# Kernel optimization log

Hardware: AMD Instinct MI355X
Metric: run time of the kernel (lower is better)

The kernel has to match this reference:

```python
import jax, jax.numpy as jnp
import numpy as np

C = 64          # in_channels (per-head channel dim)
HEADS = 8
GROUPS = 32
EPS = 1e-6
B, H, W = 8, 64, 64


def group_norm(x, gamma, beta):
    b, c, h, w = x.shape
    xg = x.reshape(b, GROUPS, c // GROUPS, h, w)
    mu = xg.mean(axis=(2, 3, 4), keepdims=True)
    var = xg.var(axis=(2, 3, 4), keepdims=True)
    xn = ((xg - mu) / jnp.sqrt(var + EPS)).reshape(b, c, h, w)
    return xn * gamma[None, :, None, None] + beta[None, :, None, None]


def conv1x1(x, wgt, bias):
    # wgt: [out_c, in_c], x: [b, in_c, h, w]
    return jnp.einsum('oc,bchw->bohw', wgt, x) + bias[None, :, None, None]


def setup_inputs() -> dict:
    key = jax.random.key(0)
    ks = jax.random.split(key, 10)
    sc_in = 1.0 / np.sqrt(C)
    sc_out = 1.0 / np.sqrt(C * HEADS)
    return {
        'x': jax.random.normal(ks[0], (B, C, H, W), dtype=jnp.float32),
        'gn_gamma': jnp.ones((C,), dtype=jnp.float32),
        'gn_beta': jnp.zeros((C,), dtype=jnp.float32),
        'Wq': jax.random.uniform(ks[1], (C * HEADS, C), jnp.float32, -sc_in, sc_in),
        'bq': jax.random.uniform(ks[2], (C * HEADS,), jnp.float32, -sc_in, sc_in),
        'Wk': jax.random.uniform(ks[3], (C * HEADS, C), jnp.float32, -sc_in, sc_in),
        'bk': jax.random.uniform(ks[4], (C * HEADS,), jnp.float32, -sc_in, sc_in),
        'Wv': jax.random.uniform(ks[5], (C * HEADS, C), jnp.float32, -sc_in, sc_in),
        'bv': jax.random.uniform(ks[6], (C * HEADS,), jnp.float32, -sc_in, sc_in),
        'Wo': jax.random.uniform(ks[7], (C, C * HEADS), jnp.float32, -sc_out, sc_out),
        'bo': jax.random.uniform(ks[8], (C,), jnp.float32, -sc_out, sc_out),
    }


def reference(x, gn_gamma, gn_beta, Wq, bq, Wk, bk, Wv, bv, Wo, bo):
    b, c, h, w = x.shape
    xn = group_norm(x, gn_gamma, gn_beta)
    # 1x1 conv projections -> [b, heads, c, h*w]
    q = conv1x1(xn, Wq, bq).reshape(b, HEADS, c, h * w)
    k = conv1x1(xn, Wk, bk).reshape(b, HEADS, c, h * w)
    v = conv1x1(xn, Wv, bv).reshape(b, HEADS, c, h * w)
    q = jax.nn.softmax(q, axis=-1)
    k = jax.nn.softmax(k, axis=-1)
    # out[b,h,c,q] = sum_k sum_p Q[b,h,p,q] K[b,h,p,k] V[b,h,c,k] / sqrt(c)
    # associativity: contract K with V first (O(hw*c^2) instead of O(hw^2*c))
    s = jnp.einsum('bhpk,bhck->bhpc', k, v)          # [b, heads, c, c]
    out = jnp.einsum('bhpq,bhpc->bhcq', q, s) / jnp.sqrt(jnp.float32(c))
    out = out.reshape(b, HEADS * c, h, w)
    return conv1x1(out, Wo, bo)
```

## Files before the change

kernel.cpp:

```cpp
#include <hip/hip_runtime.h>
#include <math.h>

#define BATCH 8
#define CH 64
#define NHEADS 8
#define NPIX 4096
#define QROWS 512

typedef __attribute__((ext_vector_type(8))) short short8v;
typedef __attribute__((ext_vector_type(16))) float f32x16;

__device__ inline float wave_sum(float v) {
#pragma unroll
    for (int off = 32; off; off >>= 1) v += __shfl_down(v, off, 64);
    return v;
}

__device__ inline void split_bf16(float f, short& h, short& l) {
    unsigned u = __float_as_uint(f);
    unsigned r = u + 0x7FFFu + ((u >> 16) & 1u);
    h = (short)(r >> 16);
    float hf = __uint_as_float(r & 0xFFFF0000u);
    float lf = f - hf;
    unsigned u2 = __float_as_uint(lf);
    unsigned r2 = u2 + 0x7FFFu + ((u2 >> 16) & 1u);
    l = (short)(r2 >> 16);
}

__device__ inline void split4(const float4 v, uint2& hi, uint2& lo) {
    short h0, h1, h2, h3, l0, l1, l2, l3;
    split_bf16(v.x, h0, l0); split_bf16(v.y, h1, l1);
    split_bf16(v.z, h2, l2); split_bf16(v.w, h3, l3);
    hi.x = (unsigned short)h0 | ((unsigned)(unsigned short)h1 << 16);
    hi.y = (unsigned short)h2 | ((unsigned)(unsigned short)h3 << 16);
    lo.x = (unsigned short)l0 | ((unsigned)(unsigned short)l1 << 16);
    lo.y = (unsigned short)l2 | ((unsigned)(unsigned short)l3 << 16);
}

__global__ __launch_bounds__(256) void gn_zero_kernel(
    const float* __restrict__ x, const float* __restrict__ gamma,
    const float* __restrict__ beta, float* __restrict__ scale, float* __restrict__ shift,
    float* __restrict__ zbase) {
    if (blockIdx.x >= 256) {
        ((float4*)zbase)[(blockIdx.x - 256) * 256 + threadIdx.x] =
            make_float4(0.f, 0.f, 0.f, 0.f);
        return;
    }
    int b = blockIdx.x >> 5, g = blockIdx.x & 31;
    const float4* p = (const float4*)(x + ((size_t)b * CH + 2 * g) * NPIX);
    float s = 0.f, ss = 0.f;
#pragma unroll
    for (int i = 0; i < 8; ++i) {
        float4 v = p[threadIdx.x + i * 256];
        s += v.x + v.y + v.z + v.w;
        ss += v.x * v.x + v.y * v.y + v.z * v.z + v.w * v.w;
    }
    s = wave_sum(s);
    ss = wave_sum(ss);
    __shared__ float rs[4], rss[4];
    int lane = threadIdx.x & 63, wv = threadIdx.x >> 6;
    if (lane == 0) { rs[wv] = s; rss[wv] = ss; }
    __syncthreads();
    if (threadIdx.x == 0) {
        s = rs[0] + rs[1] + rs[2] + rs[3];
        ss = rss[0] + rss[1] + rss[2] + rss[3];
        float mu = s * (1.f / 8192.f);
        float var = ss * (1.f / 8192.f) - mu * mu;
        float rstd = rsqrtf(var + 1e-6f);
#pragma unroll
        for (int cc = 0; cc < 2; ++cc) {
            int c = 2 * g + cc;
            float sc = rstd * gamma[c];
            scale[b * CH + c] = sc;
            shift[b * CH + c] = beta[c] - mu * sc;
        }
    }
}

__global__ __launch_bounds__(256) void gemm1_q_kernel(
    const float* __restrict__ x, const float* __restrict__ scale_all,
    const float* __restrict__ shift_all,
    const float* __restrict__ Wq, const float* __restrict__ bq,
    float* __restrict__ qkv) {
    __shared__ __align__(16) char lds[65536];
    short* As = (short*)lds;
    short* Bs = (short*)(lds + 32768);
    float* Bf = (float*)lds;

    int t = threadIdx.x;
    int b = blockIdx.z;
    int row0 = blockIdx.y * 128, pix0 = blockIdx.x * 128;

    float4 w4[8];
#pragma unroll
    for (int i = 0; i < 8; ++i) {
        int idx = t + i * 256;
        int r = idx >> 4, c4 = idx & 15;
        w4[i] = *(const float4*)(Wq + (size_t)(row0 + r) * 64 + c4 * 4);
    }
    const float* scale = scale_all + b * CH;
    const float* shift = shift_all + b * CH;
#pragma unroll
    for (int i = 0; i < 8; ++i) {
        int idx = t + i * 256;
        int c = idx >> 5, p4 = (idx & 31) * 4;
        float4 v = *(const float4*)(x + ((size_t)b * CH + c) * NPIX + pix0 + p4);
        float sc = scale[c], sh = shift[c];
        v.x = fmaf(v.x, sc, sh); v.y = fmaf(v.y, sc, sh);
        v.z = fmaf(v.z, sc, sh); v.w = fmaf(v.w, sc, sh);
        *(float4*)&Bf[c * 132 + p4] = v;
    }
    __syncthreads();
    int mypx = t & 127, chalf = t >> 7;
    float xv[32];
#pragma unroll
    for (int e = 0; e < 32; ++e) xv[e] = Bf[(chalf * 32 + e) * 132 + mypx];
    __syncthreads();
#pragma unroll
    for (int i = 0; i < 8; ++i) {
        int idx = t + i * 256;
        int r = idx >> 4, c4 = (idx & 15) * 4;
        uint2 hi, lo;
        split4(w4[i], hi, lo);
        int chh = ((c4 >> 3) ^ (r & 7));
        int chl = ((8 + (c4 >> 3)) ^ (r & 7));
        *(uint2*)&As[r * 128 + chh * 8 + (c4 & 7)] = hi;
        *(uint2*)&As[r * 128 + chl * 8 + (c4 & 7)] = lo;
    }
    {
        short h[32], l[32];
#pragma unroll
        for (int e = 0; e < 32; ++e) split_bf16(xv[e], h[e], l[e]);
#pragma unroll
        for (int w = 0; w < 4; ++w) {
            short8v hv, lv;
#pragma unroll
            for (int e = 0; e < 8; ++e) { hv[e] = h[w * 8 + e]; lv[e] = l[w * 8 + e]; }
            int chh = ((chalf * 4 + w) ^ (mypx & 7));
            int chl = ((8 + chalf * 4 + w) ^ (mypx & 7));
            *(short8v*)&Bs[mypx * 128 + chh * 8] = hv;
            *(short8v*)&Bs[mypx * 128 + chl * 8] = lv;
        }
    }
    __syncthreads();

    int lane = t & 63, wid = t >> 6;
    int wm = wid >> 1, wn = wid & 1;
    int l31 = lane & 31, l7 = lane & 7, kg = lane >> 5;
    int arow = wm * 64 + l31;
    int brow = wn * 64 + l31;
    f32x16 acc[2][2];
#pragma unroll
    for (int mt = 0; mt < 2; ++mt)
#pragma unroll
        for (int nt = 0; nt < 2; ++nt)
#pragma unroll
            for (int e = 0; e < 16; ++e) acc[mt][nt][e] = 0.f;
    const int ACH[12] = {0, 2, 4, 6, 8, 10, 12, 14, 0, 2, 4, 6};
    const int BCH[12] = {0, 2, 4, 6, 0, 2, 4, 6, 8, 10, 12, 14};
#pragma unroll
    for (int ks = 0; ks < 12; ++ks) {
        int ach = ACH[ks] + kg, bch = BCH[ks] + kg;
        short8v a0 = *(const short8v*)&As[arow * 128 + ((ach ^ l7) << 3)];
        short8v a1 = *(const short8v*)&As[(arow + 32) * 128 + ((ach ^ l7) << 3)];
        short8v b0 = *(const short8v*)&Bs[brow * 128 + ((bch ^ l7) << 3)];
        short8v b1 = *(const short8v*)&Bs[(brow + 32) * 128 + ((bch ^ l7) << 3)];
        acc[0][0] = __builtin_amdgcn_mfma_f32_32x32x16_bf16(a0, b0, acc[0][0], 0, 0, 0);
        acc[0][1] = __builtin_amdgcn_mfma_f32_32x32x16_bf16(a0, b1, acc[0][1], 0, 0, 0);
        acc[1][0] = __builtin_amdgcn_mfma_f32_32x32x16_bf16(a1, b0, acc[1][0], 0, 0, 0);
        acc[1][1] = __builtin_amdgcn_mfma_f32_32x32x16_bf16(a1, b1, acc[1][1], 0, 0, 0);
    }
#pragma unroll
    for (int mt = 0; mt < 2; ++mt) {
#pragma unroll
        for (int j = 0; j < 16; ++j) {
            int rl = wm * 64 + mt * 32 + (j & 3) + 8 * (j >> 2) + 4 * kg;
            float bi = bq[row0 + rl];
#pragma unroll
            for (int nt = 0; nt < 2; ++nt) {
                float val = __expf(acc[mt][nt][j] + bi);
                qkv[((size_t)b * QROWS + row0 + rl) * NPIX + pix0 + wn * 64 + nt * 32 + l31] = val;
            }
        }
    }
}

__global__ __launch_bounds__(256) void gemm_kv_fused_kernel(
    const float* __restrict__ x, const float* __restrict__ scale_all,
    const float* __restrict__ shift_all,
    const float* __restrict__ Wk, const float* __restrict__ bk,
    const float* __restrict__ Wv, const float* __restrict__ bv,
    float* __restrict__ sraw, float* __restrict__ ksum) {
    __shared__ __align__(16) char lds[131072];
    short* As = (short*)lds;
    short* Bs = (short*)(lds + 32768);
    short* Eh = (short*)(lds + 65536);
    short* El = (short*)(lds + 98304);
    short* Vh = (short*)lds;
    short* Vl = (short*)(lds + 32768);
    float* Bf = (float*)lds;

    int t = threadIdx.x;
    int b = blockIdx.z;
    int r = blockIdx.y;
    int pix0 = blockIdx.x * 128;

    float4 w4[8];
#pragma unroll
    for (int i = 0; i < 8; ++i) {
        int idx = t + i * 256;
        int rr = idx >> 4, c4 = idx & 15;
        w4[i] = *(const float4*)(Wk + (size_t)(r * 128 + rr) * 64 + c4 * 4);
    }
    const float* scale = scale_all + b * CH;
    const float* shift = shift_all + b * CH;
#pragma unroll
    for (int i = 0; i < 8; ++i) {
        int idx = t + i * 256;
        int c = idx >> 5, p4 = (idx & 31) * 4;
        float4 v = *(const float4*)(x + ((size_t)b * CH + c) * NPIX + pix0 + p4);
        float sc = scale[c], sh = shift[c];
        v.x = fmaf(v.x, sc, sh); v.y = fmaf(v.y, sc, sh);
        v.z = fmaf(v.z, sc, sh); v.w = fmaf(v.w, sc, sh);
        *(float4*)&Bf[c * 132 + p4] = v;
    }
    __syncthreads();
    int mypx = t & 127, chalf = t >> 7;
    float xv[32];
#pragma unroll
    for (int e = 0; e < 32; ++e) xv[e] = Bf[(chalf * 32 + e) * 132 + mypx];
    __syncthreads();
#pragma unroll
    for (int i = 0; i < 8; ++i) {
        int idx = t + i * 256;
        int rr = idx >> 4, c4 = (idx & 15) * 4;
        uint2 hi, lo;
        split4(w4[i], hi, lo);
        int chh = ((c4 >> 3) ^ (rr & 7));
        int chl = ((8 + (c4 >> 3)) ^ (rr & 7));
        *(uint2*)&As[rr * 128 + chh * 8 + (c4 & 7)] = hi;
        *(uint2*)&As[rr * 128 + chl * 8 + (c4 & 7)] = lo;
    }
    {
        short h[32], l[32];
#pragma unroll
        for (int e = 0; e < 32; ++e) split_bf16(xv[e], h[e], l[e]);
#pragma unroll
        for (int w = 0; w < 4; ++w) {
            short8v hv, lv;
#pragma unroll
            for (int e = 0; e < 8; ++e) { hv[e] = h[w * 8 + e]; lv[e] = l[w * 8 + e]; }
            int chh = ((chalf * 4 + w) ^ (mypx & 7));
            int chl = ((8 + chalf * 4 + w) ^ (mypx & 7));
            *(short8v*)&Bs[mypx * 128 + chh * 8] = hv;
            *(short8v*)&Bs[mypx * 128 + chl * 8] = lv;
        }
    }
    float4 w4v[8];
#pragma unroll
    for (int i = 0; i < 8; ++i) {
        int idx = t + i * 256;
        int rr = idx >> 4, c4 = idx & 15;
        w4v[i] = *(const float4*)(Wv + (size_t)(r * 128 + rr) * 64 + c4 * 4);
    }
    __syncthreads();

    int lane = t & 63, wid = t >> 6;
    int wm = wid >> 1, wn = wid & 1;
    int l31 = lane & 31, l7 = lane & 7, kg = lane >> 5;
    int axrow = wm * 64 + l31;
    int bwrow = wn * 64 + l31;
    const int XCH[12] = {0, 2, 4, 6, 8, 10, 12, 14, 0, 2, 4, 6};
    const int WCH[12] = {0, 2, 4, 6, 0, 2, 4, 6, 8, 10, 12, 14};

    f32x16 acc[2][2];
#pragma unroll
    for (int mt = 0; mt < 2; ++mt)
#pragma unroll
        for (int nt = 0; nt < 2; ++nt)
#pragma unroll
            for (int e = 0; e < 16; ++e) acc[mt][nt][e] = 0.f;
#pragma unroll
    for (int ks = 0; ks < 12; ++ks) {
        int xch = XCH[ks] + kg, wch = WCH[ks] + kg;
        short8v a0 = *(const short8v*)&Bs[axrow * 128 + ((xch ^ l7) << 3)];
        short8v a1 = *(const short8v*)&Bs[(axrow + 32) * 128 + ((xch ^ l7) << 3)];
        short8v b0 = *(const short8v*)&As[bwrow * 128 + ((wch ^ l7) << 3)];
        short8v b1 = *(const short8v*)&As[(bwrow + 32) * 128 + ((wch ^ l7) << 3)];
        acc[0][0] = __builtin_amdgcn_mfma_f32_32x32x16_bf16(a0, b0, acc[0][0], 0, 0, 0);
        acc[0][1] = __builtin_amdgcn_mfma_f32_32x32x16_bf16(a0, b1, acc[0][1], 0, 0, 0);
        acc[1][0] = __builtin_amdgcn_mfma_f32_32x32x16_bf16(a1, b0, acc[1][0], 0, 0, 0);
        acc[1][1] = __builtin_amdgcn_mfma_f32_32x32x16_bf16(a1, b1, acc[1][1], 0, 0, 0);
    }
#pragma unroll
    for (int nt = 0; nt < 2; ++nt) {
        int krow = wn * 64 + nt * 32 + l31;
        float bi = bk[r * 128 + krow];
        float part = 0.f;
#pragma unroll
        for (int mt = 0; mt < 2; ++mt) {
#pragma unroll
            for (int g = 0; g < 4; ++g) {
                float4 ev;
                ev.x = __expf(acc[mt][nt][g * 4 + 0] + bi);
                ev.y = __expf(acc[mt][nt][g * 4 + 1] + bi);
                ev.z = __expf(acc[mt][nt][g * 4 + 2] + bi);
                ev.w = __expf(acc[mt][nt][g * 4 + 3] + bi);
                part += ev.x + ev.y + ev.z + ev.w;
                uint2 hi, lo;
                split4(ev, hi, lo);
                int ch = wm * 8 + mt * 4 + g;
                int off = krow * 128 + ((ch ^ (krow & 7)) << 3) + 4 * kg;
                *(uint2*)&Eh[off] = hi;
                *(uint2*)&El[off] = lo;
            }
        }
        part += __shfl_xor(part, 32);
        if (kg == 0) atomicAdd(&ksum[b * 512 + r * 128 + krow], part);
    }
    __syncthreads();
#pragma unroll
    for (int i = 0; i < 8; ++i) {
        int idx = t + i * 256;
        int rr = idx >> 4, c4 = (idx & 15) * 4;
        uint2 hi, lo;
        split4(w4v[i], hi, lo);
        int chh = ((c4 >> 3) ^ (rr & 7));
        int chl = ((8 + (c4 >> 3)) ^ (rr & 7));
        *(uint2*)&As[rr * 128 + chh * 8 + (c4 & 7)] = hi;
        *(uint2*)&As[rr * 128 + chl * 8 + (c4 & 7)] = lo;
    }
    __syncthreads();
#pragma unroll
    for (int mt = 0; mt < 2; ++mt)
#pragma unroll
        for (int nt = 0; nt < 2; ++nt)
#pragma unroll
            for (int e = 0; e < 16; ++e) acc[mt][nt][e] = 0.f;
#pragma unroll
    for (int ks = 0; ks < 12; ++ks) {
        int xch = XCH[ks] + kg, wch = WCH[ks] + kg;
        short8v a0 = *(const short8v*)&Bs[axrow * 128 + ((xch ^ l7) << 3)];
        short8v a1 = *(const short8v*)&Bs[(axrow + 32) * 128 + ((xch ^ l7) << 3)];
        short8v b0 = *(const short8v*)&As[bwrow * 128 + ((wch ^ l7) << 3)];
        short8v b1 = *(const short8v*)&As[(bwrow + 32) * 128 + ((wch ^ l7) << 3)];
        acc[0][0] = __builtin_amdgcn_mfma_f32_32x32x16_bf16(a0, b0, acc[0][0], 0, 0, 0);
        acc[0][1] = __builtin_amdgcn_mfma_f32_32x32x16_bf16(a0, b1, acc[0][1], 0, 0, 0);
        acc[1][0] = __builtin_amdgcn_mfma_f32_32x32x16_bf16(a1, b0, acc[1][0], 0, 0, 0);
        acc[1][1] = __builtin_amdgcn_mfma_f32_32x32x16_bf16(a1, b1, acc[1][1], 0, 0, 0);
    }
    __syncthreads();
#pragma unroll
    for (int nt = 0; nt < 2; ++nt) {
        int vrow = wn * 64 + nt * 32 + l31;
        float bi = bv[r * 128 + vrow];
#pragma unroll
        for (int mt = 0; mt < 2; ++mt) {
#pragma unroll
            for (int g = 0; g < 4; ++g) {
                float4 vv;
                vv.x = acc[mt][nt][g * 4 + 0] + bi;
                vv.y = acc[mt][nt][g * 4 + 1] + bi;
                vv.z = acc[mt][nt][g * 4 + 2] + bi;
                vv.w = acc[mt][nt][g * 4 + 3] + bi;
                uint2 hi, lo;
                split4(vv, hi, lo);
                int ch = wm * 8 + mt * 4 + g;
                int off = vrow * 128 + ((ch ^ (vrow & 7)) << 3) + 4 * kg;
                *(uint2*)&Vh[off] = hi;
                *(uint2*)&Vl[off] = lo;
            }
        }
    }
    __syncthreads();
    int hh = wid & 1, pp = wid >> 1;
    int ar = (hh * 64 + pp * 32 + l31) * 128;
    int br0 = (hh * 64 + l31) * 128;
    int br1 = (hh * 64 + 32 + l31) * 128;
    f32x16 cacc[2];
#pragma unroll
    for (int C = 0; C < 2; ++C)
#pragma unroll
        for (int e = 0; e < 16; ++e) cacc[C][e] = 0.f;
#pragma unroll
    for (int s = 0; s < 8; ++s) {
        int ch = (((2 * s + kg) ^ l7) << 3);
        short8v a = *(const short8v*)&Eh[ar + ch];
        short8v b0 = *(const short8v*)&Vh[br0 + ch];
        short8v b1 = *(const short8v*)&Vh[br1 + ch];
        cacc[0] = __builtin_amdgcn_mfma_f32_32x32x16_bf16(a, b0, cacc[0], 0, 0, 0);
        cacc[1] = __builtin_amdgcn_mfma_f32_32x32x16_bf16(a, b1, cacc[1], 0, 0, 0);
    }
#pragma unroll
    for (int s = 0; s < 8; ++s) {
        int ch = (((2 * s + kg) ^ l7) << 3);
        short8v a = *(const short8v*)&El[ar + ch];
        short8v b0 = *(const short8v*)&Vh[br0 + ch];
        short8v b1 = *(const short8v*)&Vh[br1 + ch];
        cacc[0] = __builtin_amdgcn_mfma_f32_32x32x16_bf16(a, b0, cacc[0], 0, 0, 0);
        cacc[1] = __builtin_amdgcn_mfma_f32_32x32x16_bf16(a, b1, cacc[1], 0, 0, 0);
    }
#pragma unroll
    for (int s = 0; s < 8; ++s) {
        int ch = (((2 * s + kg) ^ l7) << 3);
        short8v a = *(const short8v*)&Eh[ar + ch];
        short8v b0 = *(const short8v*)&Vl[br0 + ch];
        short8v b1 = *(const short8v*)&Vl[br1 + ch];
        cacc[0] = __builtin_amdgcn_mfma_f32_32x32x16_bf16(a, b0, cacc[0], 0, 0, 0);
        cacc[1] = __builtin_amdgcn_mfma_f32_32x32x16_bf16(a, b1, cacc[1], 0, 0, 0);
    }
    int h = r * 2 + hh;
    float* sr = sraw + (((size_t)b * 8 + h) * 64) * 64;
#pragma unroll
    for (int C = 0; C < 2; ++C) {
#pragma unroll
        for (int j = 0; j < 16; ++j) {
            int p = pp * 32 + (j & 3) + 8 * (j >> 2) + 4 * kg;
            int c = C * 32 + l31;
            atomicAdd(&sr[p * 64 + c], cacc[C][j]);
        }
    }
}

__global__ __launch_bounds__(256) void rowsum_q_kernel(
    const float* __restrict__ qkv, float* __restrict__ qsum) {
    int b = blockIdx.x >> 9, row = blockIdx.x & 511;
    const float4* p = (const float4*)(qkv + ((size_t)b * QROWS + row) * NPIX);
    float s = 0.f;
#pragma unroll
    for (int i = 0; i < 4; ++i) {
        float4 v = p[threadIdx.x + i * 256];
        s += v.x + v.y + v.z + v.w;
    }
    s = wave_sum(s);
    __shared__ float rs[4];
    int lane = threadIdx.x & 63, wv = threadIdx.x >> 6;
    if (lane == 0) rs[wv] = s;
    __syncthreads();
    if (threadIdx.x == 0)
        qsum[b * 512 + row] = rs[0] + rs[1] + rs[2] + rs[3];
}

__global__ __launch_bounds__(256) void t_kernel(
    const float* __restrict__ sraw, const float* __restrict__ qsum_all,
    const float* __restrict__ ksum_all, const float* __restrict__ Wo, float* __restrict__ T) {
    int idx = blockIdx.x * 256 + threadIdx.x;
    int hp = idx & 511, o = (idx >> 9) & 63, b = idx >> 15;
    int h = hp >> 6, pp = hp & 63;
    const float* srow = sraw + (((size_t)b * 8 + h) * 64 + pp) * 64;
    const float* wrow = Wo + (size_t)o * 512 + h * 64;
    float acc = 0.f;
#pragma unroll
    for (int c = 0; c < 64; ++c) acc += wrow[c] * srow[c];
    float ks = ksum_all[b * 512 + hp];
    float qs = qsum_all[b * 512 + hp];
    T[idx] = acc / (8.f * ks * qs);
}

__global__ __launch_bounds__(256) void gemm2_mfma_kernel(
    const float* __restrict__ qkv, const float* __restrict__ T_all,
    const float* __restrict__ bo, float* __restrict__ out) {
    __shared__ __align__(16) short lds[16384];
    short* As = lds;
    short* Bs = lds + 8192;
    int pix0 = blockIdx.x * 64, b = blockIdx.y;
    const float* Tb = T_all + (size_t)b * 64 * 512;
    const float* qb = qkv + (size_t)b * QROWS * NPIX;
    int t = threadIdx.x;
    int lane = t & 63, wid = t >> 6;
    int wm = wid & 1, wn = wid >> 1;
    int l31 = lane & 31, l7 = lane & 7, kg = lane >> 5;
    int arow = (wm * 32 + l31) * 128;
    int brow = (wn * 32 + l31) * 128;
    int px0 = t & 63, hpq = (t >> 6) * 16;
    f32x16 acc;
#pragma unroll
    for (int e = 0; e < 16; ++e) acc[e] = 0.f;
    for (int it = 0; it < 8; ++it) {
        __syncthreads();
#pragma unroll
        for (int i = 0; i < 4; ++i) {
            int e4 = t + i * 256;
            int o = e4 >> 4, p4 = (e4 & 15) * 4;
            int chx = (((p4 >> 3) ^ (o & 7)) << 3) + (p4 & 7);
            float4 tv = *(const float4*)(Tb + (size_t)o * 512 + it * 64 + p4);
            uint2 hi, lo;
            split4(tv, hi, lo);
            *(uint2*)&As[o * 128 + chx] = hi;
            *(uint2*)&As[o * 128 + 64 + chx] = lo;
        }
        float colv[16];
#pragma unroll
        for (int e = 0; e < 16; ++e)
            colv[e] = qb[(size_t)(it * 64 + hpq + e) * NPIX + pix0 + px0];
#pragma unroll
        for (int qd = 0; qd < 4; ++qd) {
            int hpl = hpq + qd * 4;
            float4 v4 = make_float4(colv[qd * 4], colv[qd * 4 + 1],
                                    colv[qd * 4 + 2], colv[qd * 4 + 3]);
            uint2 hi, lo;
            split4(v4, hi, lo);
            int chx = (((hpl >> 3) ^ (px0 & 7)) << 3) + (hpl & 7);
            *(uint2*)&Bs[px0 * 128 + chx] = hi;
            *(uint2*)&Bs[px0 * 128 + 64 + chx] = lo;
        }
        __syncthreads();
        short8v ah[4], al[4], bh[4], bl[4];
#pragma unroll
        for (int ks = 0; ks < 4; ++ks) {
            int ch = ((ks * 2 + kg) ^ l7) << 3;
            ah[ks] = *(const short8v*)&As[arow + ch];
            al[ks] = *(const short8v*)&As[arow + 64 + ch];
            bh[ks] = *(const short8v*)&Bs[brow + ch];
            bl[ks] = *(const short8v*)&Bs[brow + 64 + ch];
        }
#pragma unroll
        for (int ks = 0; ks < 4; ++ks) {
            acc = __builtin_amdgcn_mfma_f32_32x32x16_bf16(ah[ks], bh[ks], acc, 0, 0, 0);
            acc = __builtin_amdgcn_mfma_f32_32x32x16_bf16(al[ks], bh[ks], acc, 0, 0, 0);
            acc = __builtin_amdgcn_mfma_f32_32x32x16_bf16(ah[ks], bl[ks], acc, 0, 0, 0);
        }
    }
#pragma unroll
    for (int j = 0; j < 16; ++j) {
        int o = wm * 32 + (j & 3) + 8 * (j >> 2) + 4 * kg;
        out[((size_t)b * 64 + o) * NPIX + pix0 + wn * 32 + l31] = acc[j] + bo[o];
    }
}

#define OFF_SCALE 0
#define OFF_SHIFT 512
#define OFF_QSUM  1024
#define OFF_SRAW  5120
#define OFF_KSUM  267264
#define OFF_T     271360
#define OFF_QKV   533504
#define WS_FLOATS (533504 + 16777216)

extern "C" void kernel_launch(void* const* d_in, const int* in_sizes, int n_in,
                              void* d_out, int out_size, void* d_ws, size_t ws_size,
                              hipStream_t stream) {
    const float* x  = (const float*)d_in[0];
    const float* gg = (const float*)d_in[1];
    const float* gb = (const float*)d_in[2];
    const float* Wq = (const float*)d_in[3];
    const float* bq = (const float*)d_in[4];
    const float* Wk = (const float*)d_in[5];
    const float* bk = (const float*)d_in[6];
    const float* Wv = (const float*)d_in[7];
    const float* bv = (const float*)d_in[8];
    const float* Wo = (const float*)d_in[9];
    const float* bo = (const float*)d_in[10];
    float* out = (float*)d_out;
    float* ws = (float*)d_ws;
    if (ws_size < (size_t)WS_FLOATS * sizeof(float)) return;

    float* scale = ws + OFF_SCALE;
    float* shift = ws + OFF_SHIFT;
    float* qsum  = ws + OFF_QSUM;
    float* sraw  = ws + OFF_SRAW;
    float* ksum  = ws + OFF_KSUM;
    float* T     = ws + OFF_T;
    float* qkv   = ws + OFF_QKV;

    gn_zero_kernel<<<516, 256, 0, stream>>>(x, gg, gb, scale, shift, sraw);
    gemm1_q_kernel<<<dim3(32, 4, 8), 256, 0, stream>>>(x, scale, shift, Wq, bq, qkv);
    gemm_kv_fused_kernel<<<dim3(32, 4, 8), 256, 0, stream>>>(x, scale, shift, Wk, bk, Wv, bv,
                                                             sraw, ksum);
    rowsum_q_kernel<<<4096, 256, 0, stream>>>(qkv, qsum);
    t_kernel<<<1024, 256, 0, stream>>>(sraw, qsum, ksum, Wo, T);
    gemm2_mfma_kernel<<<dim3(64, 8), 256, 0, stream>>>(qkv, T, bo, out);
}
```

Baseline: 193.3 us.

## Fuse Q row-sum into gemm1 epilogue and widen KV kernel to 512 threads

The separate rowsum_q kernel, which re-read the whole exp(Q) buffer from global memory, is removed. Row sums are now reduced with cross-lane shuffles in the gemm1 epilogue and accumulated into qsum with atomics. The zeroing kernel gets extra blocks and now zeroes qsum instead of the raw S buffer, presumably covering both regions. The fused K/V kernel moves to 512 threads with half the per-thread tile, to raise parallelism and cut register pressure. The cost is more atomics and, in that kernel, less reuse of LDS fragments per MFMA.

Result: slower. 219.9 us (+13.8%).

```diff
diff --git a/kernel.cpp b/kernel.cpp
--- a/kernel.cpp
+++ b/kernel.cpp
@@ -81,7 +81,7 @@
     const float* __restrict__ x, const float* __restrict__ scale_all,
     const float* __restrict__ shift_all,
     const float* __restrict__ Wq, const float* __restrict__ bq,
-    float* __restrict__ qkv) {
+    float* __restrict__ qkv, float* __restrict__ qsum) {
     __shared__ __align__(16) char lds[65536];
     short* As = (short*)lds;
     short* Bs = (short*)(lds + 32768);
@@ -176,16 +176,23 @@
         for (int j = 0; j < 16; ++j) {
             int rl = wm * 64 + mt * 32 + (j & 3) + 8 * (j >> 2) + 4 * kg;
             float bi = bq[row0 + rl];
-#pragma unroll
-            for (int nt = 0; nt < 2; ++nt) {
-                float val = __expf(acc[mt][nt][j] + bi);
-                qkv[((size_t)b * QROWS + row0 + rl) * NPIX + pix0 + wn * 64 + nt * 32 + l31] = val;
-            }
-        }
-    }
-}
-
-__global__ __launch_bounds__(256) void gemm_kv_fused_kernel(
+            float e0 = __expf(acc[mt][0][j] + bi);
+            float e1 = __expf(acc[mt][1][j] + bi);
+            float* o = qkv + ((size_t)b * QROWS + row0 + rl) * NPIX + pix0;
+            o[wn * 64 + l31] = e0;
+            o[wn * 64 + 32 + l31] = e1;
+            float rsum = e0 + e1;
+            rsum += __shfl_xor(rsum, 1);
+            rsum += __shfl_xor(rsum, 2);
+            rsum += __shfl_xor(rsum, 4);
+            rsum += __shfl_xor(rsum, 8);
+            rsum += __shfl_xor(rsum, 16);
+            if (l31 == 0) atomicAdd(&qsum[b * 512 + row0 + rl], rsum);
+        }
+    }
+}
+
+__global__ __launch_bounds__(512) void gemm_kv_fused_kernel(
     const float* __restrict__ x, const float* __restrict__ scale_all,
     const float* __restrict__ shift_all,
     const float* __restrict__ Wk, const float* __restrict__ bk,
@@ -205,18 +212,18 @@
     int r = blockIdx.y;
     int pix0 = blockIdx.x * 128;
 
-    float4 w4[8];
-#pragma unroll
-    for (int i = 0; i < 8; ++i) {
-        int idx = t + i * 256;
+    float4 w4[4];
+#pragma unroll
+    for (int i = 0; i < 4; ++i) {
+        int idx = t + i * 512;
         int rr = idx >> 4, c4 = idx & 15;
         w4[i] = *(const float4*)(Wk + (size_t)(r * 128 + rr) * 64 + c4 * 4);
     }
     const float* scale = scale_all + b * CH;
     const float* shift = shift_all + b * CH;
 #pragma unroll
-    for (int i = 0; i < 8; ++i) {
-        int idx = t + i * 256;
+    for (int i = 0; i < 4; ++i) {
+        int idx = t + i * 512;
         int c = idx >> 5, p4 = (idx & 31) * 4;
         float4 v = *(const float4*)(x + ((size_t)b * CH + c) * NPIX + pix0 + p4);
         float sc = scale[c], sh = shift[c];
@@ -225,14 +232,14 @@
         *(float4*)&Bf[c * 132 + p4] = v;
     }
     __syncthreads();
-    int mypx = t & 127, chalf = t >> 7;
-    float xv[32];
-#pragma unroll
-    for (int e = 0; e < 32; ++e) xv[e] = Bf[(chalf * 32 + e) * 132 + mypx];
-    __syncthreads();
-#pragma unroll
-    for (int i = 0; i < 8; ++i) {
-        int idx = t + i * 256;
+    int mypx = t & 127, cq = t >> 7;
+    float xv[16];
+#pragma unroll
+    for (int e = 0; e < 16; ++e) xv[e] = Bf[(cq * 16 + e) * 132 + mypx];
+    __syncthreads();
+#pragma unroll
+    for (int i = 0; i < 4; ++i) {
+        int idx = t + i * 512;
         int rr = idx >> 4, c4 = (idx & 15) * 4;
         uint2 hi, lo;
         split4(w4[i], hi, lo);
@@ -242,59 +249,53 @@
         *(uint2*)&As[rr * 128 + chl * 8 + (c4 & 7)] = lo;
     }
     {
-        short h[32], l[32];
-#pragma unroll
-        for (int e = 0; e < 32; ++e) split_bf16(xv[e], h[e], l[e]);
-#pragma unroll
-        for (int w = 0; w < 4; ++w) {
+        short h[16], l[16];
+#pragma unroll
+        for (int e = 0; e < 16; ++e) split_bf16(xv[e], h[e], l[e]);
+#pragma unroll
+        for (int w = 0; w < 2; ++w) {
             short8v hv, lv;
 #pragma unroll
             for (int e = 0; e < 8; ++e) { hv[e] = h[w * 8 + e]; lv[e] = l[w * 8 + e]; }
-            int chh = ((chalf * 4 + w) ^ (mypx & 7));
-            int chl = ((8 + chalf * 4 + w) ^ (mypx & 7));
+            int chh = ((cq * 2 + w) ^ (mypx & 7));
+            int chl = ((8 + cq * 2 + w) ^ (mypx & 7));
             *(short8v*)&Bs[mypx * 128 + chh * 8] = hv;
             *(short8v*)&Bs[mypx * 128 + chl * 8] = lv;
         }
     }
-    float4 w4v[8];
-#pragma unroll
-    for (int i = 0; i < 8; ++i) {
-        int idx = t + i * 256;
+    float4 w4v[4];
+#pragma unroll
+    for (int i = 0; i < 4; ++i) {
+        int idx = t + i * 512;
         int rr = idx >> 4, c4 = idx & 15;
         w4v[i] = *(const float4*)(Wv + (size_t)(r * 128 + rr) * 64 + c4 * 4);
     }
     __syncthreads();
 
     int lane = t & 63, wid = t >> 6;
-    int wm = wid >> 1, wn = wid & 1;
+    int wm = wid >> 2, wn = wid & 3;
     int l31 = lane & 31, l7 = lane & 7, kg = lane >> 5;
     int axrow = wm * 64 + l31;
-    int bwrow = wn * 64 + l31;
+    int bwrow = wn * 32 + l31;
     const int XCH[12] = {0, 2, 4, 6, 8, 10, 12, 14, 0, 2, 4, 6};
     const int WCH[12] = {0, 2, 4, 6, 0, 2, 4, 6, 8, 10, 12, 14};
 
-    f32x16 acc[2][2];
+    f32x16 acc[2];
 #pragma unroll
     for (int mt = 0; mt < 2; ++mt)
 #pragma unroll
-        for (int nt = 0; nt < 2; ++nt)
-#pragma unroll
-            for (int e = 0; e < 16; ++e) acc[mt][nt][e] = 0.f;
+        for (int e = 0; e < 16; ++e) acc[mt][e] = 0.f;
 #pragma unroll
     for (int ks = 0; ks < 12; ++ks) {
         int xch = XCH[ks] + kg, wch = WCH[ks] + kg;
         short8v a0 = *(const short8v*)&Bs[axrow * 128 + ((xch ^ l7) << 3)];
         short8v a1 = *(const short8v*)&Bs[(axrow + 32) * 128 + ((xch ^ l7) << 3)];
         short8v b0 = *(const short8v*)&As[bwrow * 128 + ((wch ^ l7) << 3)];
-        short8v b1 = *(const short8v*)&As[(bwrow + 32) * 128 + ((wch ^ l7) << 3)];
-        acc[0][0] = __builtin_amdgcn_mfma_f32_32x32x16_bf16(a0, b0, acc[0][0], 0, 0, 0);
-        acc[0][1] = __builtin_amdgcn_mfma_f32_32x32x16_bf16(a0, b1, acc[0][1], 0, 0, 0);
-        acc[1][0] = __builtin_amdgcn_mfma_f32_32x32x16_bf16(a1, b0, acc[1][0], 0, 0, 0);
-        acc[1][1] = __builtin_amdgcn_mfma_f32_32x32x16_bf16(a1, b1, acc[1][1], 0, 0, 0);
-    }
-#pragma unroll
-    for (int nt = 0; nt < 2; ++nt) {
-        int krow = wn * 64 + nt * 32 + l31;
+        acc[0] = __builtin_amdgcn_mfma_f32_32x32x16_bf16(a0, b0, acc[0], 0, 0, 0);
+        acc[1] = __builtin_amdgcn_mfma_f32_32x32x16_bf16(a1, b0, acc[1], 0, 0, 0);
+    }
+    {
+        int krow = wn * 32 + l31;
         float bi = bk[r * 128 + krow];
         float part = 0.f;
 #pragma unroll
@@ -302,10 +303,10 @@
 #pragma unroll
             for (int g = 0; g < 4; ++g) {
                 float4 ev;
-                ev.x = __expf(acc[mt][nt][g * 4 + 0] + bi);
-                ev.y = __expf(acc[mt][nt][g * 4 + 1] + bi);
-                ev.z = __expf(acc[mt][nt][g * 4 + 2] + bi);
-                ev.w = __expf(acc[mt][nt][g * 4 + 3] + bi);
+                ev.x = __expf(acc[mt][g * 4 + 0] + bi);
+                ev.y = __expf(acc[mt][g * 4 + 1] + bi);
+                ev.z = __expf(acc[mt][g * 4 + 2] + bi);
+                ev.w = __expf(acc[mt][g * 4 + 3] + bi);
                 part += ev.x + ev.y + ev.z + ev.w;
                 uint2 hi, lo;
                 split4(ev, hi, lo);
@@ -320,8 +321,8 @@
     }
     __syncthreads();
 #pragma unroll
-    for (int i = 0; i < 8; ++i) {
-        int idx = t + i * 256;
+    for (int i = 0; i < 4; ++i) {
+        int idx = t + i * 512;
         int rr = idx >> 4, c4 = (idx & 15) * 4;
         uint2 hi, lo;
         split4(w4v[i], hi, lo);
@@ -334,35 +335,29 @@
 #pragma unroll
     for (int mt = 0; mt < 2; ++mt)
 #pragma unroll
-        for (int nt = 0; nt < 2; ++nt)
-#pragma unroll
-            for (int e = 0; e < 16; ++e) acc[mt][nt][e] = 0.f;
+        for (int e = 0; e < 16; ++e) acc[mt][e] = 0.f;
 #pragma unroll
     for (int ks = 0; ks < 12; ++ks) {
         int xch = XCH[ks] + kg, wch = WCH[ks] + kg;
         short8v a0 = *(const short8v*)&Bs[axrow * 128 + ((xch ^ l7) << 3)];
         short8v a1 = *(const short8v*)&Bs[(axrow + 32) * 128 + ((xch ^ l7) << 3)];
         short8v b0 = *(const short8v*)&As[bwrow * 128 + ((wch ^ l7) << 3)];
-        short8v b1 = *(const short8v*)&As[(bwrow + 32) * 128 + ((wch ^ l7) << 3)];
-        acc[0][0] = __builtin_amdgcn_mfma_f32_32x32x16_bf16(a0, b0, acc[0][0], 0, 0, 0);
-        acc[0][1] = __builtin_amdgcn_mfma_f32_32x32x16_bf16(a0, b1, acc[0][1], 0, 0, 0);
-        acc[1][0] = __builtin_amdgcn_mfma_f32_32x32x16_bf16(a1, b0, acc[1][0], 0, 0, 0);
-        acc[1][1] = __builtin_amdgcn_mfma_f32_32x32x16_bf16(a1, b1, acc[1][1], 0, 0, 0);
-    }
-    __syncthreads();
-#pragma unroll
-    for (int nt = 0; nt < 2; ++nt) {
-        int vrow = wn * 64 + nt * 32 + l31;
+        acc[0] = __builtin_amdgcn_mfma_f32_32x32x16_bf16(a0, b0, acc[0], 0, 0, 0);
+        acc[1] = __builtin_amdgcn_mfma_f32_32x32x16_bf16(a1, b0, acc[1], 0, 0, 0);
+    }
+    __syncthreads();
+    {
+        int vrow = wn * 32 + l31;
         float bi = bv[r * 128 + vrow];
 #pragma unroll
         for (int mt = 0; mt < 2; ++mt) {
 #pragma unroll
             for (int g = 0; g < 4; ++g) {
                 float4 vv;
-                vv.x = acc[mt][nt][g * 4 + 0] + bi;
-                vv.y = acc[mt][nt][g * 4 + 1] + bi;
-                vv.z = acc[mt][nt][g * 4 + 2] + bi;
-                vv.w = acc[mt][nt][g * 4 + 3] + bi;
+                vv.x = acc[mt][g * 4 + 0] + bi;
+                vv.y = acc[mt][g * 4 + 1] + bi;
+                vv.z = acc[mt][g * 4 + 2] + bi;
+                vv.w = acc[mt][g * 4 + 3] + bi;
                 uint2 hi, lo;
                 split4(vv, hi, lo);
                 int ch = wm * 8 + mt * 4 + g;
@@ -373,72 +368,42 @@
         }
     }
     __syncthreads();
-    int hh = wid & 1, pp = wid >> 1;
+    int hh = wid >> 2, pc = wid & 3;
+    int pp = pc >> 1, cc = pc & 1;
     int ar = (hh * 64 + pp * 32 + l31) * 128;
-    int br0 = (hh * 64 + l31) * 128;
-    int br1 = (hh * 64 + 32 + l31) * 128;
-    f32x16 cacc[2];
-#pragma unroll
-    for (int C = 0; C < 2; ++C)
-#pragma unroll
-        for (int e = 0; e < 16; ++e) cacc[C][e] = 0.f;
+    int br = (hh * 64 + cc * 32 + l31) * 128;
+    f32x16 cacc;
+#pragma unroll
+    for (int e = 0; e < 16; ++e) cacc[e] = 0.f;
 #pragma unroll
     for (int s = 0; s < 8; ++s) {
         int ch = (((2 * s + kg) ^ l7) << 3);
         short8v a = *(const short8v*)&Eh[ar + ch];
-        short8v b0 = *(const short8v*)&Vh[br0 + ch];
-        short8v b1 = *(const short8v*)&Vh[br1 + ch];
-        cacc[0] = __builtin_amdgcn_mfma_f32_32x32x16_bf16(a, b0, cacc[0], 0, 0, 0);
-        cacc[1] = __builtin_amdgcn_mfma_f32_32x32x16_bf16(a, b1, cacc[1], 0, 0, 0);
+        short8v bb = *(const short8v*)&Vh[br + ch];
+        cacc = __builtin_amdgcn_mfma_f32_32x32x16_bf16(a, bb, cacc, 0, 0, 0);
     }
 #pragma unroll
     for (int s = 0; s < 8; ++s) {
         int ch = (((2 * s + kg) ^ l7) << 3);
         short8v a = *(const short8v*)&El[ar + ch];
-        short8v b0 = *(const short8v*)&Vh[br0 + ch];
-        short8v b1 = *(const short8v*)&Vh[br1 + ch];
-        cacc[0] = __builtin_amdgcn_mfma_f32_32x32x16_bf16(a, b0, cacc[0], 0, 0, 0);
-        cacc[1] = __builtin_amdgcn_mfma_f32_32x32x16_bf16(a, b1, cacc[1], 0, 0, 0);
+        short8v bb = *(const short8v*)&Vh[br + ch];
+        cacc = __builtin_amdgcn_mfma_f32_32x32x16_bf16(a, bb, cacc, 0, 0, 0);
     }
 #pragma unroll
     for (int s = 0; s < 8; ++s) {
         int ch = (((2 * s + kg) ^ l7) << 3);
         short8v a = *(const short8v*)&Eh[ar + ch];
-        short8v b0 = *(const short8v*)&Vl[br0 + ch];
-        short8v b1 = *(const short8v*)&Vl[br1 + ch];
-        cacc[0] = __builtin_amdgcn_mfma_f32_32x32x16_bf16(a, b0, cacc[0], 0, 0, 0);
-        cacc[1] = __builtin_amdgcn_mfma_f32_32x32x16_bf16(a, b1, cacc[1], 0, 0, 0);
+        short8v bb = *(const short8v*)&Vl[br + ch];
+        cacc = __builtin_amdgcn_mfma_f32_32x32x16_bf16(a, bb, cacc, 0, 0, 0);
     }
     int h = r * 2 + hh;
     float* sr = sraw + (((size_t)b * 8 + h) * 64) * 64;
 #pragma unroll
-    for (int C = 0; C < 2; ++C) {
-#pragma unroll
-        for (int j = 0; j < 16; ++j) {
-            int p = pp * 32 + (j & 3) + 8 * (j >> 2) + 4 * kg;
-            int c = C * 32 + l31;
-            atomicAdd(&sr[p * 64 + c], cacc[C][j]);
-        }
-    }
-}
-
-__global__ __launch_bounds__(256) void rowsum_q_kernel(
-    const float* __restrict__ qkv, float* __restrict__ qsum) {
-    int b = blockIdx.x >> 9, row = blockIdx.x & 511;
-    const float4* p = (const float4*)(qkv + ((size_t)b * QROWS + row) * NPIX);
-    float s = 0.f;
-#pragma unroll
-    for (int i = 0; i < 4; ++i) {
-        float4 v = p[threadIdx.x + i * 256];
-        s += v.x + v.y + v.z + v.w;
-    }
-    s = wave_sum(s);
-    __shared__ float rs[4];
-    int lane = threadIdx.x & 63, wv = threadIdx.x >> 6;
-    if (lane == 0) rs[wv] = s;
-    __syncthreads();
-    if (threadIdx.x == 0)
-        qsum[b * 512 + row] = rs[0] + rs[1] + rs[2] + rs[3];
+    for (int j = 0; j < 16; ++j) {
+        int p = pp * 32 + (j & 3) + 8 * (j >> 2) + 4 * kg;
+        int c = cc * 32 + l31;
+        atomicAdd(&sr[p * 64 + c], cacc[j]);
+    }
 }
 
 __global__ __launch_bounds__(256) void t_kernel(
@@ -563,11 +528,10 @@
     float* T     = ws + OFF_T;
     float* qkv   = ws + OFF_QKV;
 
-    gn_zero_kernel<<<516, 256, 0, stream>>>(x, gg, gb, scale, shift, sraw);
-    gemm1_q_kernel<<<dim3(32, 4, 8), 256, 0, stream>>>(x, scale, shift, Wq, bq, qkv);
-    gemm_kv_fused_kernel<<<dim3(32, 4, 8), 256, 0, stream>>>(x, scale, shift, Wk, bk, Wv, bv,
+    gn_zero_kernel<<<520, 256, 0, stream>>>(x, gg, gb, scale, shift, qsum);
+    gemm1_q_kernel<<<dim3(32, 4, 8), 256, 0, stream>>>(x, scale, shift, Wq, bq, qkv, qsum);
+    gemm_kv_fused_kernel<<<dim3(32, 4, 8), 512, 0, stream>>>(x, scale, shift, Wk, bk, Wv, bv,
                                                              sraw, ksum);
-    rowsum_q_kernel<<<4096, 256, 0, stream>>>(qkv, qsum);
     t_kernel<<<1024, 256, 0, stream>>>(sraw, qsum, ksum, Wo, T);
     gemm2_mfma_kernel<<<dim3(64, 8), 256, 0, stream>>>(qkv, T, bo, out);
 }
```
